# Kernel tuning notes

Measured on AMD Instinct MI355X. Metric: run time of the kernel, lower is better.

## Reference

```python
import jax, jax.numpy as jnp
import numpy as np

N, IN, OUT, T = 500000, 128, 64, 8

def setup_inputs() -> dict:
    key = jax.random.key(0)
    k1, k2, k3, k4 = jax.random.split(key, 4)
    x = jax.random.normal(k1, (N, IN), dtype=jnp.float32)
    node_type = jax.random.randint(k2, (N,), 0, T, dtype=jnp.int32)
    # per-type Linear weights, stored as [T, IN, OUT] so x @ W[t] matches torch Linear
    W = jax.random.normal(k3, (T, IN, OUT), dtype=jnp.float32) * (1.0 / np.sqrt(IN))
    b = jax.random.normal(k4, (T, OUT), dtype=jnp.float32) * 0.01
    return {"x": x, "node_type": node_type, "W": W, "b": b}

def reference(x, node_type, W, b):
    # emb_x[mask_t] = x[mask_t] @ W[t] + b[t], for each node type t.
    # Vectorized: loop over the small fixed number of types, masked accumulate.
    T_ = W.shape[0]
    out = jnp.zeros((x.shape[0], W.shape[2]), dtype=x.dtype)
    for t in range(T_):
        y_t = x @ W[t] + b[t]                      # [N, OUT]
        mask = (node_type == t)[:, None]           # [N, 1]
        out = jnp.where(mask, y_t, out)
    return out
```

## Files before the change

### kernel.cpp

```cpp
#include <hip/hip_runtime.h>
#include <hip/hip_bf16.h>

#define NT   8
#define INF  128
#define OUTF 64
#define BR   128

typedef __attribute__((ext_vector_type(8))) short short8;
typedef __attribute__((ext_vector_type(4))) short short4v;
typedef __attribute__((ext_vector_type(4))) float f32x4;

__device__ __forceinline__ short f2bf(float f) {
  __hip_bfloat16 h = __float2bfloat16(f);
  return __builtin_bit_cast(short, h);
}

__global__ void hl_wconv(const float* __restrict__ W, short* __restrict__ wbf) {
  const int tid   = blockIdx.x * blockDim.x + threadIdx.x;
  const int combo = tid >> 6;
  const int lane  = tid & 63;
  const int t = combo >> 4, s = (combo >> 2) & 3, nb = combo & 3;
  const int q = lane >> 4, c = lane & 15;
  const float* Wt = W + t * INF * OUTF;
  short8 v;
  #pragma unroll
  for (int j = 0; j < 8; ++j)
    v[j] = f2bf(Wt[(s * 32 + q * 8 + j) * OUTF + nb * 16 + c]);
  *(short8*)(wbf + (size_t)tid * 8) = v;
}

__global__ __launch_bounds__(256, 4) void hl_lb(
    const float* __restrict__ x, const int* __restrict__ nty,
    const short* __restrict__ wbf, const float* __restrict__ b,
    float* __restrict__ out, int N) {
  __shared__ short xs[BR * 128];
  __shared__ int lcnt[NT], cbase[NT];
  __shared__ int lorder[BR];
  __shared__ int descs[16];
  __shared__ int ndesc;

  const int tid   = threadIdx.x;
  const int base  = blockIdx.x * BR;
  const int nrows = min(BR, N - base);

  if (tid < NT) lcnt[tid] = 0;
  __syncthreads();

  const int nf4 = nrows * 32;
  for (int f4 = tid; f4 < nf4; f4 += 256) {
    const int row = f4 >> 5, q4 = f4 & 31;
    f32x4 v = *(const f32x4*)(x + (size_t)(base + row) * INF + q4 * 4);
    short4v s4;
    s4[0] = f2bf(v[0]); s4[1] = f2bf(v[1]);
    s4[2] = f2bf(v[2]); s4[3] = f2bf(v[3]);
    const int byt = (q4 * 8) ^ ((row & 7) << 4);
    *(short4v*)((char*)xs + row * 256 + byt) = s4;
  }

  int myrank = 0, myty = 0;
  if (tid < nrows) {
    myty = nty[base + tid];
    myrank = atomicAdd(&lcnt[myty], 1);
  }
  __syncthreads();

  if (tid == 0) {
    int o = 0, nd = 0;
    #pragma unroll
    for (int t = 0; t < NT; ++t) {
      cbase[t] = o;
      const int cn = lcnt[t];
      for (int j = 0; j < cn; j += 16) {
        const int valid = min(16, cn - j);
        descs[nd++] = t | (valid << 3) | ((o + j) << 8);
      }
      o += cn;
    }
    ndesc = nd;
  }
  __syncthreads();
  if (tid < nrows) lorder[cbase[myty] + myrank] = tid;
  __syncthreads();

  const int wave = tid >> 6, lane = tid & 63;
  const int q = lane >> 4, c = lane & 15;
  const int nd = ndesc;
  const short* wp = wbf + lane * 8;

  for (int i = wave; i < nd; i += 4) {
    const int d = descs[i];
    const int t = d & 7, valid = (d >> 3) & 31, loff = d >> 8;

    const int am   = c < valid ? c : valid - 1;
    const int lrow = lorder[loff + am];
    const char* arow = (const char*)xs + lrow * 256;
    const int sw = (lrow & 7) << 4;
    short8 A[4];
    #pragma unroll
    for (int s = 0; s < 4; ++s)
      A[s] = *(const short8*)(arow + ((s * 64 + q * 16) ^ sw));

    f32x4 acc[4];
    #pragma unroll
    for (int nb = 0; nb < 4; ++nb) acc[nb] = (f32x4){0, 0, 0, 0};

    #pragma unroll
    for (int s = 0; s < 4; ++s) {
      #pragma unroll
      for (int nb = 0; nb < 4; ++nb) {
        short8 B = *(const short8*)(wp + (size_t)(((t * 4 + s) * 4 + nb)) * 512);
        acc[nb] = __builtin_amdgcn_mfma_f32_16x16x32_bf16(A[s], B, acc[nb], 0, 0, 0);
      }
    }

    float bv[4];
    #pragma unroll
    for (int nb = 0; nb < 4; ++nb) bv[nb] = b[t * OUTF + nb * 16 + c];
    #pragma unroll
    for (int r = 0; r < 4; ++r) {
      const int m = q * 4 + r;
      if (m < valid) {
        const int grow = base + lorder[loff + m];
        float* orow = out + (size_t)grow * OUTF + c;
        #pragma unroll
        for (int nb = 0; nb < 4; ++nb)
          orow[nb * 16] = acc[nb][r] + bv[nb];
      }
    }
  }
}

extern "C" void kernel_launch(void* const* d_in, const int* in_sizes, int n_in,
                              void* d_out, int out_size, void* d_ws, size_t ws_size,
                              hipStream_t stream) {
  const float* x  = (const float*)d_in[0];
  const int*   nt = (const int*)d_in[1];
  const float* W  = (const float*)d_in[2];
  const float* b  = (const float*)d_in[3];
  float* out = (float*)d_out;
  const int N = in_sizes[1];
  short* wbf = (short*)d_ws;

  hl_wconv<<<32, 256, 0, stream>>>(W, wbf);
  const int gb = (N + BR - 1) / BR;
  hl_lb<<<gb, 256, 0, stream>>>(x, nt, wbf, b, out, N);
}
```

Measured before the change: 412.8 us.

## Drop LDS staging of x; gather rows directly from global per tile

After: 424.6 us. 1.03x slower.

```diff
diff --git a/kernel.cpp b/kernel.cpp
--- a/kernel.cpp
+++ b/kernel.cpp
@@ -4,10 +4,9 @@
 #define NT   8
 #define INF  128
 #define OUTF 64
-#define BR   128
+#define BR   256
 
 typedef __attribute__((ext_vector_type(8))) short short8;
-typedef __attribute__((ext_vector_type(4))) short short4v;
 typedef __attribute__((ext_vector_type(4))) float f32x4;
 
 __device__ __forceinline__ short f2bf(float f) {
@@ -29,57 +28,44 @@
   *(short8*)(wbf + (size_t)tid * 8) = v;
 }
 
-__global__ __launch_bounds__(256, 4) void hl_lb(
+__global__ __launch_bounds__(256, 4) void hl_nb(
     const float* __restrict__ x, const int* __restrict__ nty,
     const short* __restrict__ wbf, const float* __restrict__ b,
     float* __restrict__ out, int N) {
-  __shared__ short xs[BR * 128];
   __shared__ int lcnt[NT], cbase[NT];
-  __shared__ int lorder[BR];
-  __shared__ int descs[16];
+  __shared__ short lorder[BR];
+  __shared__ int descs[NT + BR / 16];
   __shared__ int ndesc;
 
   const int tid   = threadIdx.x;
   const int base  = blockIdx.x * BR;
   const int nrows = min(BR, N - base);
 
+  int myty = 0;
+  if (tid < nrows) myty = nty[base + tid];
   if (tid < NT) lcnt[tid] = 0;
   __syncthreads();
-
-  const int nf4 = nrows * 32;
-  for (int f4 = tid; f4 < nf4; f4 += 256) {
-    const int row = f4 >> 5, q4 = f4 & 31;
-    f32x4 v = *(const f32x4*)(x + (size_t)(base + row) * INF + q4 * 4);
-    short4v s4;
-    s4[0] = f2bf(v[0]); s4[1] = f2bf(v[1]);
-    s4[2] = f2bf(v[2]); s4[3] = f2bf(v[3]);
-    const int byt = (q4 * 8) ^ ((row & 7) << 4);
-    *(short4v*)((char*)xs + row * 256 + byt) = s4;
+  int myrank = 0;
+  if (tid < nrows) myrank = atomicAdd(&lcnt[myty], 1);
+  __syncthreads();
+  if (tid < NT) {
+    int o = 0;
+    #pragma unroll
+    for (int t = 0; t < NT; ++t) o += (t < tid) ? lcnt[t] : 0;
+    cbase[tid] = o;
   }
-
-  int myrank = 0, myty = 0;
-  if (tid < nrows) {
-    myty = nty[base + tid];
-    myrank = atomicAdd(&lcnt[myty], 1);
-  }
-  __syncthreads();
-
   if (tid == 0) {
-    int o = 0, nd = 0;
-    #pragma unroll
+    int nd = 0, o = 0;
     for (int t = 0; t < NT; ++t) {
-      cbase[t] = o;
       const int cn = lcnt[t];
-      for (int j = 0; j < cn; j += 16) {
-        const int valid = min(16, cn - j);
-        descs[nd++] = t | (valid << 3) | ((o + j) << 8);
-      }
+      for (int j = 0; j < cn; j += 16)
+        descs[nd++] = t | (min(16, cn - j) << 3) | ((o + j) << 8);
       o += cn;
     }
     ndesc = nd;
   }
   __syncthreads();
-  if (tid < nrows) lorder[cbase[myty] + myrank] = tid;
+  if (tid < nrows) lorder[cbase[myty] + myrank] = (short)tid;
   __syncthreads();
 
   const int wave = tid >> 6, lane = tid & 63;
@@ -93,12 +79,17 @@
 
     const int am   = c < valid ? c : valid - 1;
     const int lrow = lorder[loff + am];
-    const char* arow = (const char*)xs + lrow * 256;
-    const int sw = (lrow & 7) << 4;
+    const float* xr = x + (size_t)(base + lrow) * INF;
     short8 A[4];
     #pragma unroll
-    for (int s = 0; s < 4; ++s)
-      A[s] = *(const short8*)(arow + ((s * 64 + q * 16) ^ sw));
+    for (int s = 0; s < 4; ++s) {
+      f32x4 v0 = *(const f32x4*)(xr + s * 32 + q * 8);
+      f32x4 v1 = *(const f32x4*)(xr + s * 32 + q * 8 + 4);
+      short8 a;
+      #pragma unroll
+      for (int j = 0; j < 4; ++j) { a[j] = f2bf(v0[j]); a[j + 4] = f2bf(v1[j]); }
+      A[s] = a;
+    }
 
     f32x4 acc[4];
     #pragma unroll
@@ -108,7 +99,7 @@
     for (int s = 0; s < 4; ++s) {
       #pragma unroll
       for (int nb = 0; nb < 4; ++nb) {
-        short8 B = *(const short8*)(wp + (size_t)(((t * 4 + s) * 4 + nb)) * 512);
+        short8 B = *(const short8*)(wp + (size_t)((t * 4 + s) * 4 + nb) * 512);
         acc[nb] = __builtin_amdgcn_mfma_f32_16x16x32_bf16(A[s], B, acc[nb], 0, 0, 0);
       }
     }
@@ -143,5 +134,5 @@
 
   hl_wconv<<<32, 256, 0, stream>>>(W, wbf);
   const int gb = (N + BR - 1) / BR;
-  hl_lb<<<gb, 256, 0, stream>>>(x, nt, wbf, b, out, N);
+  hl_nb<<<gb, 256, 0, stream>>>(x, nt, wbf, b, out, N);
 }
```
